# Kernel tuning notes

Measured on AMD Instinct MI355X. Metric: run time of the kernel, lower is better.

The kernel has to match this reference:

```python
import jax, jax.numpy as jnp
import numpy as np

D_MODEL = 1024
NUM_HEADS = 16
HEAD_DIM = D_MODEL // NUM_HEADS
B, S = 4, 2048


def setup_inputs() -> dict:
    key = jax.random.key(0)
    ks = jax.random.split(key, 11)
    sc = 1.0 / np.sqrt(D_MODEL)
    return {
        "query": jax.random.normal(ks[0], (B, S, D_MODEL), jnp.float32),
        "key": jax.random.normal(ks[1], (B, S, D_MODEL), jnp.float32),
        "value": jax.random.normal(ks[2], (B, S, D_MODEL), jnp.float32),
        "Wq": jax.random.normal(ks[3], (D_MODEL, D_MODEL), jnp.float32) * sc,
        "bq": jnp.zeros((D_MODEL,), jnp.float32),
        "Wk": jax.random.normal(ks[4], (D_MODEL, D_MODEL), jnp.float32) * sc,
        "bk": jnp.zeros((D_MODEL,), jnp.float32),
        "Wv": jax.random.normal(ks[5], (D_MODEL, D_MODEL), jnp.float32) * sc,
        "bv": jnp.zeros((D_MODEL,), jnp.float32),
        "Wo": jax.random.normal(ks[6], (D_MODEL, D_MODEL), jnp.float32) * sc,
        "bo": jnp.zeros((D_MODEL,), jnp.float32),
    }


def _split_heads(x):
    b, s, _ = x.shape
    return x.reshape(b, s, NUM_HEADS, HEAD_DIM).transpose(0, 2, 1, 3)  # [B,H,S,Dh]


def reference(query, key, value, Wq, bq, Wk, bk, Wv, bv, Wo, bo):
    q = _split_heads(query @ Wq + bq)
    k = _split_heads(key @ Wk + bk)
    v = _split_heads(value @ Wv + bv)
    scores = jnp.einsum("bhqd,bhkd->bhqk", q, k) / np.sqrt(HEAD_DIM)
    attn = jax.nn.softmax(scores, axis=-1)
    out = jnp.einsum("bhqk,bhkd->bhqd", attn, v)
    out = out.transpose(0, 2, 1, 3).reshape(query.shape[0], -1, D_MODEL)
    return out @ Wo + bo
```

## Files before the change

kernel.cpp:

```cpp
#include <hip/hip_runtime.h>

typedef unsigned short u16;
typedef unsigned int   u32;
typedef unsigned long long u64;
typedef __attribute__((ext_vector_type(8))) short bf16x8;
typedef __attribute__((ext_vector_type(4))) float f32x4;

#define S_  2048
#define DH  64
#define DM  1024
#define BS  8192
#define CS  0.18033688011112042f

static __device__ __forceinline__ float bf2f(u16 v){ return __uint_as_float(((u32)v)<<16); }
static __device__ __forceinline__ u16 f2bf(float f){
  u32 x = __float_as_uint(f);
  return (u16)((x + 0x7fffu + ((x>>16)&1u)) >> 16);
}
#if __has_builtin(__builtin_amdgcn_cvt_pk_bf16_f32)
static __device__ __forceinline__ u32 pk2(float x, float y){
  typedef __attribute__((ext_vector_type(2))) __bf16 bf2v;
  union { bf2v v; u32 u; } c; c.v = __builtin_amdgcn_cvt_pk_bf16_f32(x, y); return c.u;
}
#else
static __device__ __forceinline__ u32 pk2(float x, float y){
  return (u32)f2bf(x) | ((u32)f2bf(y) << 16);
}
#endif
#if __has_builtin(__builtin_amdgcn_exp2f)
#define EXP2F(x) __builtin_amdgcn_exp2f(x)
#else
#define EXP2F(x) exp2f(x)
#endif

static __device__ __forceinline__ void dma16(const u16* g, const u16* l){
  __builtin_amdgcn_global_load_lds(
      (const __attribute__((address_space(1))) u32*)(u64)(uintptr_t)g,
      (__attribute__((address_space(3))) u32*)(u32)(u64)(uintptr_t)l, 16, 0, 0);
}

static __device__ __forceinline__ bf16x8 lds_frag(const u16* p){
  union { bf16x8 f; uint2 u[2]; } w;
  w.u[0] = *(const uint2*)(p);
  w.u[1] = *(const uint2*)(p+4);
  return w.f;
}
static __device__ __forceinline__ bf16x8 frag16v(const u16* p){
  union { bf16x8 f; uint4 u; } w;
  w.u = *(const uint4*)p;
  return w.f;
}
static __device__ __forceinline__ void stage16_bf(const u16* __restrict__ g, u16* s){
  uint4 a = *(const uint4*)g;
  uint4 b = *(const uint4*)(g+8);
  *(uint2*)(s+0)  = make_uint2(a.x,a.y);
  *(uint2*)(s+4)  = make_uint2(a.z,a.w);
  *(uint2*)(s+8)  = make_uint2(b.x,b.y);
  *(uint2*)(s+12) = make_uint2(b.z,b.w);
}
static __device__ __forceinline__ void stage16_f32(const float* __restrict__ g, u16* s){
  float4 a0 = ((const float4*)g)[0];
  float4 a1 = ((const float4*)g)[1];
  float4 a2 = ((const float4*)g)[2];
  float4 a3 = ((const float4*)g)[3];
  *(uint2*)(s+0)  = make_uint2(pk2(a0.x,a0.y), pk2(a0.z,a0.w));
  *(uint2*)(s+4)  = make_uint2(pk2(a1.x,a1.y), pk2(a1.z,a1.w));
  *(uint2*)(s+8)  = make_uint2(pk2(a2.x,a2.y), pk2(a2.z,a2.w));
  *(uint2*)(s+12) = make_uint2(pk2(a3.x,a3.y), pk2(a3.z,a3.w));
}

union AFU { bf16x8 f; u32 u[4]; };

__global__ __launch_bounds__(256) void prep(
    const void* __restrict__ w0, const void* __restrict__ w1,
    const void* __restrict__ w2, const void* __restrict__ w3,
    u16* t0, u16* t1, u16* t2, u16* t3,
    const void* __restrict__ a0, const void* __restrict__ a1,
    const void* __restrict__ a2,
    u16* c0, u16* c1, u16* c2, const int f32f){
  __shared__ u16 tile[32][33];
  int z = blockIdx.z;
  int tid = threadIdx.x;
  bool f32 = f32f != 0;
  if (z < 4){
    const void* in = z==0?w0 : z==1?w1 : z==2?w2 : w3;
    u16* out = z==0?t0 : z==1?t1 : z==2?t2 : t3;
    int tx = tid & 31, ty = tid >> 5;
    int c  = blockIdx.x*32 + tx;
    int r0 = blockIdx.y*32;
    for (int i=ty;i<32;i+=8){
      long off = (long)(r0+i)*DM + c;
      tile[i][tx] = f32 ? f2bf(((const float*)in)[off]) : ((const u16*)in)[off];
    }
    __syncthreads();
    int rr = r0 + tx, cb = blockIdx.x*32;
    for (int i=ty;i<32;i+=8) out[(long)(cb+i)*DM + rr] = tile[tx][i];
  } else {
    if (!f32) return;
    const void* in = z==4?a0 : z==5?a1 : a2;
    u16* out = z==4?c0 : z==5?c1 : c2;
    long lb = (long)blockIdx.y*32 + blockIdx.x;
    long base = (lb*256 + tid)*8;
    #pragma unroll
    for (int it=0; it<4; it++){
      long i = base + (long)it*2097152;
      const float4* p = (const float4*)((const float*)in + i);
      float4 x = p[0], y = p[1];
      *(uint4*)(out + i) = make_uint4(pk2(x.x,x.y), pk2(x.z,x.w), pk2(y.x,y.y), pk2(y.z,y.w));
    }
  }
}

template<int ADMA>
__global__ __launch_bounds__(256) void gemm_qkv(
    const void* __restrict__ A0, const void* __restrict__ A1, const void* __restrict__ A2,
    const u16* __restrict__ W0, const u16* __restrict__ W1, const u16* __restrict__ W2,
    const void* __restrict__ bv0, const void* __restrict__ bv1, const void* __restrict__ bv2,
    u16* C0, u16* C1, u16* C2, const int f32f){
  constexpr int AST = ADMA ? 32 : 36;
  constexpr int NB  = ADMA ? 2 : 1;
  __shared__ __align__(16) u16 As[NB][128*AST];
  __shared__ __align__(16) u16 Bs[NB][128*32];
  int z = blockIdx.z;
  const void* A  = z==0?A0 : z==1?A1 : A2;
  const u16* BT  = z==0?W0 : z==1?W1 : W2;
  const void* bias = z==0?bv0 : z==1?bv1 : bv2;
  u16* C = z==0?C0 : z==1?C1 : C2;
  const bool aF32 = (!ADMA) && (f32f != 0);
  const bool bF32 = (f32f != 0);
  int tid = threadIdx.x;
  int by = blockIdx.x, bx = blockIdx.y;
  int lane = tid & 63, w = tid >> 6;
  int t = lane & 15, q = lane >> 4;
  int wr = w >> 1, wc = w & 1;
  f32x4 acc[4][4];
  #pragma unroll
  for(int i=0;i<4;i++) for(int j=0;j<4;j++) for(int k=0;k<4;k++) acc[i][j][k]=0.f;

  const u16* gB = BT + ((long)(bx*128 + w*32 + (lane>>2))*DM + (lane&3)*8);

  if constexpr (ADMA){
    const u16* gA = (const u16*)A + ((long)(by*128 + w*32 + (lane>>2))*DM + (lane&3)*8);
    const int lb = (w*32)*32;
    dma16(gA,         &As[0][lb]);
    dma16(gA + 16*DM, &As[0][lb + 16*32]);
    dma16(gB,         &Bs[0][lb]);
    dma16(gB + 16*DM, &Bs[0][lb + 16*32]);
    for (int k0=0; k0<DM; k0+=32){
      int cur = (k0>>5)&1;
      if (k0+32 < DM){
        dma16(gA + k0+32,         &As[cur^1][lb]);
        dma16(gA + k0+32 + 16*DM, &As[cur^1][lb + 16*32]);
        dma16(gB + k0+32,         &Bs[cur^1][lb]);
        dma16(gB + k0+32 + 16*DM, &Bs[cur^1][lb + 16*32]);
        asm volatile("s_waitcnt vmcnt(4)" ::: "memory");
      } else {
        asm volatile("s_waitcnt vmcnt(0)" ::: "memory");
      }
      __builtin_amdgcn_s_barrier();
      bf16x8 af[4], bfr[4];
      const u16* Ar = &As[cur][(wr*64 + t)*32 + q*8];
      const u16* Br = &Bs[cur][(wc*64 + t)*32 + q*8];
      #pragma unroll
      for (int rt=0;rt<4;rt++) af[rt]  = frag16v(Ar + rt*16*32);
      #pragma unroll
      for (int ct=0;ct<4;ct++) bfr[ct] = frag16v(Br + ct*16*32);
      #pragma unroll
      for (int rt=0;rt<4;rt++)
        #pragma unroll
        for (int ct=0;ct<4;ct++)
          acc[rt][ct] = __builtin_amdgcn_mfma_f32_16x16x32_bf16(af[rt], bfr[ct], acc[rt][ct], 0,0,0);
      __builtin_amdgcn_s_barrier();
    }
  } else {
    long aoff = (long)(by*128 + (tid>>1))*DM + (tid&1)*16;
    const u16* ArdB = &As[0][(wr*64 + t)*AST + q*8];
    const u16* BrdB = &Bs[0][(wc*64 + t)*32  + q*8];
    for (int k0=0; k0<DM; k0+=32){
      dma16(gB + k0,         &Bs[0][(w*32)*32]);
      dma16(gB + 16*DM + k0, &Bs[0][(w*32)*32 + 16*32]);
      u16* AsW = &As[0][(tid>>1)*36 + (tid&1)*16];
      if (aF32) stage16_f32((const float*)A + aoff + k0, AsW);
      else      stage16_bf ((const u16*)A  + aoff + k0, AsW);
      __syncthreads();
      bf16x8 af[4], bfr[4];
      #pragma unroll
      for (int rt=0;rt<4;rt++) af[rt]  = lds_frag(ArdB + rt*16*AST);
      #pragma unroll
      for (int ct=0;ct<4;ct++) bfr[ct] = lds_frag(BrdB + ct*16*32);
      #pragma unroll
      for (int rt=0;rt<4;rt++)
        #pragma unroll
        for (int ct=0;ct<4;ct++)
          acc[rt][ct] = __builtin_amdgcn_mfma_f32_16x16x32_bf16(af[rt], bfr[ct], acc[rt][ct], 0,0,0);
      __syncthreads();
    }
  }

  float scale = (z==0) ? CS : 1.0f;
  #pragma unroll
  for (int ct=0;ct<4;ct++){
    int col = bx*128 + wc*64 + ct*16 + t;
    float bvv = bF32 ? ((const float*)bias)[col] : bf2f(((const u16*)bias)[col]);
    #pragma unroll
    for (int rt=0;rt<4;rt++){
      int row0 = by*128 + wr*64 + rt*16 + q*4;
      if (z == 2){
        int bb = row0 >> 11, s = row0 & 2047;
        long vbase = (long)bb*2097152 + (long)col*2048
                   + (s & ~63) + ((rt>>1)<<5) + (q<<3) + ((rt&1)<<2);
        u32 lo = pk2(acc[rt][ct][0]+bvv, acc[rt][ct][1]+bvv);
        u32 hi = pk2(acc[rt][ct][2]+bvv, acc[rt][ct][3]+bvv);
        *(uint2*)(C + vbase) = make_uint2(lo,hi);
      } else {
        #pragma unroll
        for (int r=0;r<4;r++)
          C[(long)(row0+r)*DM + col] = f2bf((acc[rt][ct][r] + bvv)*scale);
      }
    }
  }
}

__global__ __launch_bounds__(256) void gemm_o(const u16* __restrict__ A,
    const u16* __restrict__ BT, const void* __restrict__ bias, void* __restrict__ C,
    const int f32f){
  __shared__ __align__(16) u16 As[2][128*32];
  __shared__ __align__(16) u16 Bs[2][128*32];
  const int f = f32f;
  int tid = threadIdx.x;
  int by = blockIdx.x, bx = blockIdx.y;
  int lane = tid & 63, w = tid >> 6;
  int t = lane & 15, q = lane >> 4;
  int wr = w >> 1, wc = w & 1;
  f32x4 acc[4][4];
  #pragma unroll
  for(int i=0;i<4;i++) for(int j=0;j<4;j++) for(int k=0;k<4;k++) acc[i][j][k]=0.f;

  const u16* gA = A  + ((long)(by*128 + w*32 + (lane>>2))*DM + (lane&3)*8);
  const u16* gB = BT + ((long)(bx*128 + w*32 + (lane>>2))*DM + (lane&3)*8);
  const int lb = (w*32)*32;
  dma16(gA,         &As[0][lb]);
  dma16(gA + 16*DM, &As[0][lb + 16*32]);
  dma16(gB,         &Bs[0][lb]);
  dma16(gB + 16*DM, &Bs[0][lb + 16*32]);
  for (int k0=0; k0<DM; k0+=32){
    int cur = (k0>>5)&1;
    if (k0+32 < DM){
      dma16(gA + k0+32,         &As[cur^1][lb]);
      dma16(gA + k0+32 + 16*DM, &As[cur^1][lb + 16*32]);
      dma16(gB + k0+32,         &Bs[cur^1][lb]);
      dma16(gB + k0+32 + 16*DM, &Bs[cur^1][lb + 16*32]);
      asm volatile("s_waitcnt vmcnt(4)" ::: "memory");
    } else {
      asm volatile("s_waitcnt vmcnt(0)" ::: "memory");
    }
    __builtin_amdgcn_s_barrier();
    bf16x8 af[4], bfr[4];
    const u16* Ar = &As[cur][(wr*64 + t)*32 + q*8];
    const u16* Br = &Bs[cur][(wc*64 + t)*32 + q*8];
    #pragma unroll
    for (int rt=0;rt<4;rt++) af[rt]  = frag16v(Ar + rt*16*32);
    #pragma unroll
    for (int ct=0;ct<4;ct++) bfr[ct] = frag16v(Br + ct*16*32);
    #pragma unroll
    for (int rt=0;rt<4;rt++)
      #pragma unroll
      for (int ct=0;ct<4;ct++)
        acc[rt][ct] = __builtin_amdgcn_mfma_f32_16x16x32_bf16(af[rt], bfr[ct], acc[rt][ct], 0,0,0);
    __builtin_amdgcn_s_barrier();
  }
  #pragma unroll
  for (int ct=0;ct<4;ct++){
    int col = bx*128 + wc*64 + ct*16 + t;
    float bvv = f ? ((const float*)bias)[col] : bf2f(((const u16*)bias)[col]);
    #pragma unroll
    for (int rt=0;rt<4;rt++){
      int row0 = by*128 + wr*64 + rt*16 + q*4;
      #pragma unroll
      for (int r=0;r<4;r++){
        long idx = (long)(row0+r)*DM + col;
        float v = acc[rt][ct][r] + bvv;
        if (f) ((float*)C)[idx] = v;
        else   ((u16*)C)[idx]  = f2bf(v);
      }
    }
  }
}

static __device__ __forceinline__ void qk16(const u16* Kc, int t, int q, int xorv,
    const bf16x8 (&qf)[2][2], f32x4 (&sacc)[2][4]){
  #pragma unroll
  for (int i=0;i<2;i++)
    #pragma unroll
    for (int j=0;j<4;j++)
      #pragma unroll
      for (int k=0;k<4;k++) sacc[i][j][k]=0.f;
  #pragma unroll
  for (int ks=0; ks<2; ks++){
    int off = ((ks*64 + q*16) ^ xorv) >> 1;
    bf16x8 k0 = frag16v(Kc + (t     )*64 + off);
    bf16x8 k1 = frag16v(Kc + (16 + t)*64 + off);
    bf16x8 k2 = frag16v(Kc + (32 + t)*64 + off);
    bf16x8 k3 = frag16v(Kc + (48 + t)*64 + off);
    __builtin_amdgcn_s_setprio(1);
    #pragma unroll
    for (int rt=0; rt<2; rt++){
      sacc[rt][0] = __builtin_amdgcn_mfma_f32_16x16x32_bf16(k0, qf[rt][ks], sacc[rt][0],0,0,0);
      sacc[rt][1] = __builtin_amdgcn_mfma_f32_16x16x32_bf16(k1, qf[rt][ks], sacc[rt][1],0,0,0);
      sacc[rt][2] = __builtin_amdgcn_mfma_f32_16x16x32_bf16(k2, qf[rt][ks], sacc[rt][2],0,0,0);
      sacc[rt][3] = __builtin_amdgcn_mfma_f32_16x16x32_bf16(k3, qf[rt][ks], sacc[rt][3],0,0,0);
    }
    __builtin_amdgcn_s_setprio(0);
  }
}

static __device__ __forceinline__ void sm16(const f32x4 (&sacc)[2][4], AFU (&af)[2][2]){
  #pragma unroll
  for (int rt=0; rt<2; rt++){
    float ev[4][4];
    #pragma unroll
    for (int c=0; c<4; c++)
      #pragma unroll
      for (int r=0; r<4; r++) ev[c][r] = EXP2F(sacc[rt][c][r]);
    #pragma unroll
    for (int ks=0; ks<2; ks++){
      af[rt][ks].u[0] = pk2(ev[2*ks  ][0], ev[2*ks  ][1]);
      af[rt][ks].u[1] = pk2(ev[2*ks  ][2], ev[2*ks  ][3]);
      af[rt][ks].u[2] = pk2(ev[2*ks+1][0], ev[2*ks+1][1]);
      af[rt][ks].u[3] = pk2(ev[2*ks+1][2], ev[2*ks+1][3]);
    }
  }
}

static __device__ __forceinline__ void pv16(const u16* Vc, int t, int q, int xorv,
    const AFU (&af)[2][2], bf16x8 vonef, f32x4 (&o)[2][4], f32x4 (&o4)[2]){
  #pragma unroll
  for (int ks=0; ks<2; ks++){
    int off = ((ks*64 + q*16) ^ xorv) >> 1;
    bf16x8 v0 = frag16v(Vc + (t     )*64 + off);
    bf16x8 v1 = frag16v(Vc + (16 + t)*64 + off);
    bf16x8 v2 = frag16v(Vc + (32 + t)*64 + off);
    bf16x8 v3 = frag16v(Vc + (48 + t)*64 + off);
    __builtin_amdgcn_s_setprio(1);
    #pragma unroll
    for (int rt=0; rt<2; rt++){
      o[rt][0] = __builtin_amdgcn_mfma_f32_16x16x32_bf16(af[rt][ks].f, v0, o[rt][0],0,0,0);
      o[rt][1] = __builtin_amdgcn_mfma_f32_16x16x32_bf16(af[rt][ks].f, v1, o[rt][1],0,0,0);
      o[rt][2] = __builtin_amdgcn_mfma_f32_16x16x32_bf16(af[rt][ks].f, v2, o[rt][2],0,0,0);
      o[rt][3] = __builtin_amdgcn_mfma_f32_16x16x32_bf16(af[rt][ks].f, v3, o[rt][3],0,0,0);
      o4[rt]   = __builtin_amdgcn_mfma_f32_16x16x32_bf16(af[rt][ks].f, vonef, o4[rt],0,0,0);
    }
    __builtin_amdgcn_s_setprio(0);
  }
}

__global__ __launch_bounds__(256,4) void attn6(const u16* __restrict__ Q,
    const u16* __restrict__ Kb, const u16* __restrict__ Vt, u16* __restrict__ O){
  __shared__ __align__(16) u16 SM_[20480];
  const int VB = 12288;
  int tid = threadIdx.x;
  int bid = blockIdx.x;
  int qt = bid >> 6;
  int s6 = bid & 63;
  int bh = (s6 & 7)*8 + (s6 >> 3);
  int b = bh >> 4, h = bh & 15;
  int lane = tid & 63, w = tid >> 6;
  int t = lane & 15, q = lane >> 4;

  const u16* Qbase = Q + ((long)(b*S_ + qt*128 + w*32 + t)*DM + h*DH + q*8);
  bf16x8 qf[2][2];
  qf[0][0] = frag16v(Qbase);
  qf[0][1] = frag16v(Qbase + 32);
  qf[1][0] = frag16v(Qbase + 16*DM);
  qf[1][1] = frag16v(Qbase + 16*DM + 32);

  int r0 = tid >> 3;
  int cb = ((tid & 7) * 16) ^ ((r0 & 7) << 4);
  const char* gK = (const char*)Kb + (((long)(b*S_ + r0)*DM + h*DH) << 1) + cb;
  const char* gV = (const char*)Vt + ((((long)bh << 17) + ((long)r0 << 11)) << 1) + cb;
  const long gK1 = ((long)32*DM) << 1;
  const long gV1 = ((long)32*S_) << 1;
  const long KT  = ((long)64*DM) << 1;
  const int ld0 = w*512, ld1 = 2048 + w*512;

  f32x4 o[2][4];
  #pragma unroll
  for (int i=0;i<2;i++)
    #pragma unroll
    for (int j=0;j<4;j++)
      #pragma unroll
      for (int k=0;k<4;k++) o[i][j][k]=0.f;
  f32x4 o4[2];
  #pragma unroll
  for (int i=0;i<2;i++)
    #pragma unroll
    for (int k=0;k<4;k++) o4[i][k]=0.f;

  union { bf16x8 f; u32 u[4]; } vone;
  { u32 ovv = (t==0) ? 0x3F803F80u : 0u;
    vone.u[0]=ovv; vone.u[1]=ovv; vone.u[2]=ovv; vone.u[3]=ovv; }

  const int xorv = (t & 7) << 4;

  dma16((const u16*)(gK),            &SM_[ld0]);
  dma16((const u16*)(gK + gK1),      &SM_[ld1]);
  dma16((const u16*)(gV),            &SM_[VB + ld0]);
  dma16((const u16*)(gV + gV1),      &SM_[VB + ld1]);
  dma16((const u16*)(gK + KT),       &SM_[4096 + ld0]);
  dma16((const u16*)(gK + KT + gK1), &SM_[4096 + ld1]);
  asm volatile("s_waitcnt vmcnt(4)" ::: "memory");
  __builtin_amdgcn_s_barrier();

  f32x4 sacc[2][4];
  AFU af[2][2];
  qk16(&SM_[0], t, q, xorv, qf, sacc);
  sm16(sacc, af);
  dma16((const u16*)(gK + 2*KT),       &SM_[8192 + ld0]);
  dma16((const u16*)(gK + 2*KT + gK1), &SM_[8192 + ld1]);
  dma16((const u16*)(gV + (1L<<7)),        &SM_[VB + 4096 + ld0]);
  dma16((const u16*)(gV + (1L<<7) + gV1),  &SM_[VB + 4096 + ld1]);

  int kcur = 4096, knx = 8192, kfree = 0;
  for (int kt = 1; kt < 32; kt++){
    asm volatile("s_waitcnt vmcnt(4)" ::: "memory");
    __builtin_amdgcn_s_barrier();
    if (kt <= 30){
      int nk = (kt+2 < 32) ? (kt+2) : 31;
      const char* g = gK + (long)nk*KT;
      dma16((const u16*)(g),       &SM_[kfree + ld0]);
      dma16((const u16*)(g + gK1), &SM_[kfree + ld1]);
    }
    qk16(&SM_[kcur], t, q, xorv, qf, sacc);
    pv16(&SM_[VB + (((kt-1)&1)<<12)], t, q, xorv, af, vone.f, o, o4);
    sm16(sacc, af);
    __builtin_amdgcn_s_barrier();
    if (kt <= 30){
      const char* g = gV + ((long)(kt+1) << 7);
      dma16((const u16*)(g),       &SM_[VB + (((kt+1)&1)<<12) + ld0]);
      dma16((const u16*)(g + gV1), &SM_[VB + (((kt+1)&1)<<12) + ld1]);
    }
    int tmp = kcur; kcur = knx; knx = kfree; kfree = tmp;
  }
  asm volatile("s_waitcnt vmcnt(0)" ::: "memory");
  __builtin_amdgcn_s_barrier();
  pv16(&SM_[VB + 4096], t, q, xorv, af, vone.f, o, o4);

  #pragma unroll
  for (int rt=0; rt<2; rt++){
    #pragma unroll
    for (int r=0; r<4; r++){
      float l = __shfl(o4[rt][r], lane & 48);
      float inv = 1.f / l;
      int row = qt*128 + w*32 + rt*16 + q*4 + r;
      #pragma unroll
      for (int ct=0; ct<4; ct++)
        O[(long)(b*S_ + row)*DM + h*DH + ct*16 + t] = f2bf(o[rt][ct][r] * inv);
    }
  }
}

extern "C" void kernel_launch(void* const* d_in, const int* in_sizes, int n_in,
                              void* d_out, int out_size, void* d_ws, size_t ws_size,
                              hipStream_t stream){
  (void)n_in; (void)out_size;
  const void* xq = d_in[0];
  const void* xk = d_in[1];
  const void* xv = d_in[2];
  const void* Wq = d_in[3];
  const void* bq = d_in[4];
  const void* Wk = d_in[5];
  const void* bk = d_in[6];
  const void* Wv = d_in[7];
  const void* bv = d_in[8];
  const void* Wo = d_in[9];
  const void* bo = d_in[10];

  const long NT = (long)BS*DM;
  int f32f = 1;
  if (in_sizes && in_sizes[0] == (int)(NT*2)) f32f = 0;

  u16* base = (u16*)((char*)d_ws + 256);
  u16* Qb  = base;
  u16* Kbf = base + NT;
  u16* Vt  = base + 2*NT;
  u16* WqT = base + 3*NT;
  u16* WkT = WqT + (long)DM*DM;
  u16* WvT = WkT + (long)DM*DM;
  u16* WoT = WvT + (long)DM*DM;
  u16* Xc0 = WoT + (long)DM*DM;
  u16* Xc1 = Xc0 + NT;
  u16* Xc2 = Xc1 + NT;
  size_t need_pre = 256 + (size_t)(6*NT + 4*(long)DM*DM)*2;
  bool pre = ws_size >= need_pre;

  dim3 gb(256,1,1);
  int nz = (pre && f32f) ? 7 : 4;
  prep<<<dim3(32,32,nz), gb, 0, stream>>>(Wq, Wk, Wv, Wo,
      WqT, WkT, WvT, WoT, xq, xk, xv, Xc0, Xc1, Xc2, f32f);

  if (pre){
    const void* Aq = f32f ? (const void*)Xc0 : xq;
    const void* Ak = f32f ? (const void*)Xc1 : xk;
    const void* Av = f32f ? (const void*)Xc2 : xv;
    gemm_qkv<1><<<dim3(64,8,3), gb, 0, stream>>>(Aq, Ak, Av,
        WqT, WkT, WvT, bq, bk, bv, Qb, Kbf, Vt, f32f);
  } else {
    gemm_qkv<0><<<dim3(64,8,3), gb, 0, stream>>>(xq, xk, xv,
        WqT, WkT, WvT, bq, bk, bv, Qb, Kbf, Vt, f32f);
  }

  attn6<<<dim3(1024,1,1), gb, 0, stream>>>(Qb, Kbf, Vt, Qb );

  gemm_o<<<dim3(64,8,1), gb, 0, stream>>>(Qb, WoT, bo, d_out, f32f);
}
```

Baseline: 375.1 us.

## Rebalance attention K/V buffering to one barrier per tile iteration

The attention kernel's shared-memory ring changes from three K buffers and two V buffers to two K buffers and three V buffers. The next K and V tiles are now issued together at the top of each iteration, which removes the second barrier and the separate V prefetch that came after the softmax. The aim is less synchronisation stall per key tile. In exchange, the K prefetch distance drops from two tiles to one, so K load latency is less hidden.

```diff
diff --git a/kernel.cpp b/kernel.cpp
--- a/kernel.cpp
+++ b/kernel.cpp
@@ -354,10 +354,9 @@
   }
 }
 
-__global__ __launch_bounds__(256,4) void attn6(const u16* __restrict__ Q,
+__global__ __launch_bounds__(256,4) void attn7(const u16* __restrict__ Q,
     const u16* __restrict__ Kb, const u16* __restrict__ Vt, u16* __restrict__ O){
   __shared__ __align__(16) u16 SM_[20480];
-  const int VB = 12288;
   int tid = threadIdx.x;
   int bid = blockIdx.x;
   int qt = bid >> 6;
@@ -402,48 +401,44 @@
 
   const int xorv = (t & 7) << 4;
 
-  dma16((const u16*)(gK),            &SM_[ld0]);
-  dma16((const u16*)(gK + gK1),      &SM_[ld1]);
-  dma16((const u16*)(gV),            &SM_[VB + ld0]);
-  dma16((const u16*)(gV + gV1),      &SM_[VB + ld1]);
-  dma16((const u16*)(gK + KT),       &SM_[4096 + ld0]);
-  dma16((const u16*)(gK + KT + gK1), &SM_[4096 + ld1]);
-  asm volatile("s_waitcnt vmcnt(4)" ::: "memory");
+  dma16((const u16*)(gK),              &SM_[ld0]);
+  dma16((const u16*)(gK + gK1),        &SM_[ld1]);
+  dma16((const u16*)(gV),              &SM_[ 8192 + ld0]);
+  dma16((const u16*)(gV + gV1),        &SM_[ 8192 + ld1]);
+  dma16((const u16*)(gK + KT),         &SM_[ 4096 + ld0]);
+  dma16((const u16*)(gK + KT + gK1),   &SM_[ 4096 + ld1]);
+  dma16((const u16*)(gV + (1L<<7)),        &SM_[12288 + ld0]);
+  dma16((const u16*)(gV + (1L<<7) + gV1),  &SM_[12288 + ld1]);
+  asm volatile("s_waitcnt vmcnt(6)" ::: "memory");
   __builtin_amdgcn_s_barrier();
 
   f32x4 sacc[2][4];
   AFU af[2][2];
   qk16(&SM_[0], t, q, xorv, qf, sacc);
   sm16(sacc, af);
-  dma16((const u16*)(gK + 2*KT),       &SM_[8192 + ld0]);
-  dma16((const u16*)(gK + 2*KT + gK1), &SM_[8192 + ld1]);
-  dma16((const u16*)(gV + (1L<<7)),        &SM_[VB + 4096 + ld0]);
-  dma16((const u16*)(gV + (1L<<7) + gV1),  &SM_[VB + 4096 + ld1]);
-
-  int kcur = 4096, knx = 8192, kfree = 0;
+
+  int ka = 4096, kb = 0;
+  int va = 8192, vb = 12288, vc = 16384;
   for (int kt = 1; kt < 32; kt++){
-    asm volatile("s_waitcnt vmcnt(4)" ::: "memory");
+    asm volatile("s_waitcnt vmcnt(2)" ::: "memory");
     __builtin_amdgcn_s_barrier();
     if (kt <= 30){
-      int nk = (kt+2 < 32) ? (kt+2) : 31;
-      const char* g = gK + (long)nk*KT;
-      dma16((const u16*)(g),       &SM_[kfree + ld0]);
-      dma16((const u16*)(g + gK1), &SM_[kfree + ld1]);
-    }
-    qk16(&SM_[kcur], t, q, xorv, qf, sacc);
-    pv16(&SM_[VB + (((kt-1)&1)<<12)], t, q, xorv, af, vone.f, o, o4);
+      const char* g = gK + (long)(kt+1)*KT;
+      dma16((const u16*)(g),       &SM_[kb + ld0]);
+      dma16((const u16*)(g + gK1), &SM_[kb + ld1]);
+      const char* gv2 = gV + ((long)(kt+1) << 7);
+      dma16((const u16*)(gv2),       &SM_[vc + ld0]);
+      dma16((const u16*)(gv2 + gV1), &SM_[vc + ld1]);
+    }
+    qk16(&SM_[ka], t, q, xorv, qf, sacc);
+    pv16(&SM_[va], t, q, xorv, af, vone.f, o, o4);
     sm16(sacc, af);
-    __builtin_amdgcn_s_barrier();
-    if (kt <= 30){
-      const char* g = gV + ((long)(kt+1) << 7);
-      dma16((const u16*)(g),       &SM_[VB + (((kt+1)&1)<<12) + ld0]);
-      dma16((const u16*)(g + gV1), &SM_[VB + (((kt+1)&1)<<12) + ld1]);
-    }
-    int tmp = kcur; kcur = knx; knx = kfree; kfree = tmp;
+    int tk = ka; ka = kb; kb = tk;
+    int tv = va; va = vb; vb = vc; vc = tv;
   }
   asm volatile("s_waitcnt vmcnt(0)" ::: "memory");
   __builtin_amdgcn_s_barrier();
-  pv16(&SM_[VB + 4096], t, q, xorv, af, vone.f, o, o4);
+  pv16(&SM_[va], t, q, xorv, af, vone.f, o, o4);
 
   #pragma unroll
   for (int rt=0; rt<2; rt++){
@@ -509,7 +504,7 @@
         WqT, WkT, WvT, bq, bk, bv, Qb, Kbf, Vt, f32f);
   }
 
-  attn6<<<dim3(1024,1,1), gb, 0, stream>>>(Qb, Kbf, Vt, Qb );
+  attn7<<<dim3(1024,1,1), gb, 0, stream>>>(Qb, Kbf, Vt, Qb );
 
   gemm_o<<<dim3(64,8,1), gb, 0, stream>>>(Qb, WoT, bo, d_out, f32f);
 }
```

After: 387.2 us. 1.03x slower.
